# Kernel optimization log

Hardware: AMD Instinct MI355X
Metric: run time of the kernel (lower is better)

The kernel has to match this reference:

```python
import jax, jax.numpy as jnp
import numpy as np

B, S, D = 8, 2048, 768
DK = 768
OUT = 10
EPS = 1e-5

def _layernorm(x, w, b):
    mu = jnp.mean(x, axis=-1, keepdims=True)
    var = jnp.mean(jnp.square(x - mu), axis=-1, keepdims=True)
    return (x - mu) * jax.lax.rsqrt(var + EPS) * w + b

def setup_inputs() -> dict:
    key = jax.random.key(0)
    ks = jax.random.split(key, 8)
    sc_in = 1.0 / np.sqrt(D)
    sc_k = 1.0 / np.sqrt(DK)
    return {
        "src": jax.random.normal(ks[0], (B, S, D), dtype=jnp.float32),
        # weights stored as [in, out] so y = x @ W (equivalent to torch x @ W.T)
        "Wq": jax.random.uniform(ks[1], (D, DK), jnp.float32, -sc_in, sc_in),
        "Wk": jax.random.uniform(ks[2], (D, DK), jnp.float32, -sc_in, sc_in),
        "Wv": jax.random.uniform(ks[3], (D, DK), jnp.float32, -sc_in, sc_in),
        "Wo": jax.random.uniform(ks[4], (DK, D), jnp.float32, -sc_k, sc_k),
        "bo": jnp.zeros((D,), jnp.float32),
        "ln1_w": jnp.ones((D,), jnp.float32),
        "ln1_b": jnp.zeros((D,), jnp.float32),
        "ln2_w": jnp.ones((D,), jnp.float32),
        "ln2_b": jnp.zeros((D,), jnp.float32),
        "Wc": jax.random.uniform(ks[5], (D, OUT), jnp.float32, -sc_in, sc_in),
        "bc": jnp.zeros((OUT,), jnp.float32),
    }

def reference(src, Wq, Wk, Wv, Wo, bo, ln1_w, ln1_b, ln2_w, ln2_b, Wc, bc):
    # Attention (dropout in eval mode -> identity)
    Q = src @ Wq  # [B,S,DK]
    K = src @ Wk
    V = src @ Wv
    scores = jnp.einsum('bsd,btd->bst', Q, K) * (DK ** -0.5)
    attn = jax.nn.softmax(scores, axis=-1)
    out = jnp.einsum('bst,btd->bsd', attn, V) @ Wo + bo
    x = src + out
    x = _layernorm(x, ln1_w, ln1_b)
    x = _layernorm(x, ln2_w, ln2_b)
    pooled = jnp.mean(x, axis=1)  # [B,D]
    logits = pooled @ Wc + bc     # [B,OUT]
    return (logits, x)
```

## Files before the change

### kernel.cpp

```cpp
#include <hip/hip_runtime.h>
#include <cmath>

typedef unsigned short ushort_t;
typedef __bf16 bf16x8 __attribute__((ext_vector_type(8)));
typedef float  f32x4  __attribute__((ext_vector_type(4)));

#define B_  8
#define S_  2048
#define D_  768
#define MROWS (B_ * S_)
#define EPS 1e-5f
#define LDST 40

__device__ __forceinline__ float b2f(ushort_t u) {
    union { unsigned int i; float f; } v; v.i = ((unsigned int)u) << 16; return v.f;
}
__device__ __forceinline__ ushort_t f2b(float f) {
    union { float f; unsigned int i; } v; v.f = f;
    unsigned int r = v.i + 0x7fffu + ((v.i >> 16) & 1u);
    return (ushort_t)(r >> 16);
}

__device__ __forceinline__ void gload16(const ushort_t* g, ushort_t* l) {
    __builtin_amdgcn_global_load_lds((__attribute__((address_space(1))) void*)g,
                                     (__attribute__((address_space(3))) void*)l,
                                     16, 0, 0);
}

__global__ void cast_f32_bf16(const float* __restrict__ in, ushort_t* __restrict__ outp, long n)
{
    const long i = ((long)blockIdx.x * 256 + threadIdx.x) * 4;
    if (i + 3 < n) {
        const float4 v = *(const float4*)(in + i);
        ushort4 o;
        o.x = f2b(v.x); o.y = f2b(v.y); o.z = f2b(v.z); o.w = f2b(v.w);
        *(ushort4*)(outp + i) = o;
    }
}

template<int F32IN>
__global__ void transpose_any(const void* __restrict__ srcv, ushort_t* __restrict__ dst,
                              int R, int C, long sb, long db)
{
    __shared__ ushort_t tile[64 * 65];
    dst += (long)blockIdx.z * db;
    const int r0 = blockIdx.y * 64, c0 = blockIdx.x * 64;
    const int t = threadIdx.x;
    const int tr = t >> 6, tc = t & 63;
    #pragma unroll
    for (int i = 0; i < 16; i++) {
        const int r = i * 4 + tr;
        ushort_t v;
        if (F32IN) v = f2b(((const float*)srcv + (long)blockIdx.z * sb)[(long)(r0 + r) * C + (c0 + tc)]);
        else       v = ((const ushort_t*)srcv + (long)blockIdx.z * sb)[(long)(r0 + r) * C + (c0 + tc)];
        tile[r * 65 + tc] = v;
    }
    __syncthreads();
    #pragma unroll
    for (int i = 0; i < 16; i++) {
        const int r = i * 4 + tr;
        dst[(long)(c0 + r) * R + (r0 + tc)] = tile[tc * 65 + r];
    }
}


__device__ __forceinline__ void stage_half256(const ushort_t* __restrict__ g, int row0,
                                              int Kd, int k0, ushort_t* l, int tid)
{
    #pragma unroll
    for (int i = 0; i < 2; i++) {
        const int c   = i * 512 + tid;
        const int row = c >> 3;
        const int scol = ((c & 7) ^ (row & 7)) * 8;
        gload16(g + (long)(row0 + row) * Kd + (k0 + scol), l + c * 8);
    }
}

#define G256_BAR() do { \
    asm volatile("" ::: "memory"); \
    __builtin_amdgcn_s_barrier(); \
    asm volatile("" ::: "memory"); \
} while (0)

#define G256_LGKM0() asm volatile("s_waitcnt lgkmcnt(0)" ::: "memory")

#define G256_READ_A(q) do { \
    _Pragma("unroll") \
    for (int m2 = 0; m2 < 2; m2++) { \
        _Pragma("unroll") \
        for (int s = 0; s < 2; s++) { \
            int lb = (((q) * 2 + m2) * 16 + r16) * 128 + s * 64 + kq * 16; \
            lb ^= ((lb >> 7) & 7) << 4; \
            af[m2][s] = *reinterpret_cast<const bf16x8*>(LAc + (lb >> 1)); \
        } \
    } \
} while (0)

#define G256_MFMA(q) do { \
    __builtin_amdgcn_s_setprio(1); \
    _Pragma("unroll") \
    for (int m2 = 0; m2 < 2; m2++) { \
        _Pragma("unroll") \
        for (int ni = 0; ni < 4; ni++) { \
            acc[(q) * 2 + m2][ni] = __builtin_amdgcn_mfma_f32_16x16x32_bf16(af[m2][0], bg[ni][0], acc[(q) * 2 + m2][ni], 0, 0, 0); \
            acc[(q) * 2 + m2][ni] = __builtin_amdgcn_mfma_f32_16x16x32_bf16(af[m2][1], bg[ni][1], acc[(q) * 2 + m2][ni], 0, 0, 0); \
        } \
    } \
    __builtin_amdgcn_s_setprio(0); \
} while (0)

template<int MODE>
__global__ __launch_bounds__(512, 2)
void gemm256(const ushort_t* __restrict__ A, const ushort_t* __restrict__ Bt,
             void* __restrict__ Cv, int M, int N, int Kd,
             long batchA, long batchB, long batchC, float scale,
             const float* __restrict__ bias, const float* __restrict__ resid,
             float* __restrict__ rowsum)
{
    __shared__ __align__(16) ushort_t lds[65536];

    const int bz = blockIdx.z;
    A  += (long)bz * batchA;
    Bt += (long)bz * batchB;

    const int nxt  = gridDim.x;
    const int nblk = nxt * gridDim.y;
    int lin = blockIdx.y * nxt + blockIdx.x;
    if ((nblk & 7) == 0) {
        const int per = nblk >> 3;
        lin = (lin & 7) * per + (lin >> 3);
    }
    const int tile_n = (lin % nxt) * 256;
    const int tile_m = (lin / nxt) * 256;

    const int tid  = threadIdx.x;
    const int w    = tid >> 6;
    const int lane = tid & 63;
    const int wr   = w >> 2;
    const int wc   = w & 3;
    const int r16  = lane & 15;
    const int kq   = lane >> 4;
    const int brow = (wc & 1) * 64;

    const int NT = Kd >> 6;

    ushort_t* const sA = lds;
    ushort_t* const sB = lds + 16384;
    const ushort_t* const LA0 = lds + wr * 8192;
    const ushort_t* const LB0 = lds + 16384 + (wc >> 1) * 8192;

    f32x4 acc[8][4] = {};

    stage_half256(A,  tile_m,       Kd, 0,  sA,         tid);
    stage_half256(A,  tile_m + 128, Kd, 0,  sA + 8192,  tid);
    stage_half256(Bt, tile_n,       Kd, 0,  sB,         tid);
    stage_half256(Bt, tile_n + 128, Kd, 0,  sB + 8192,  tid);
    if (NT > 1) {
        stage_half256(Bt, tile_n,       Kd, 64, sB + 32768,        tid);
        stage_half256(Bt, tile_n + 128, Kd, 64, sB + 32768 + 8192, tid);
        asm volatile("s_waitcnt vmcnt(4)" ::: "memory");
    } else {
        asm volatile("s_waitcnt vmcnt(0)" ::: "memory");
    }
    G256_BAR();

    int cur = 0;
    for (int t = 0; t < NT; ++t) {
        const int k0 = t << 6;
        const ushort_t* LAc = LA0 + cur * 32768;
        const ushort_t* LBc = LB0 + cur * 32768;
        ushort_t* const nA  = sA + (cur ^ 1) * 32768;
        ushort_t* const nB  = sB + cur * 32768;

        bf16x8 bg[4][2], af[2][2];

        #pragma unroll
        for (int ni = 0; ni < 4; ni++)
            #pragma unroll
            for (int s = 0; s < 2; s++) {
                int lb = (brow + ni * 16 + r16) * 128 + s * 64 + kq * 16;
                lb ^= ((lb >> 7) & 7) << 4;
                bg[ni][s] = *reinterpret_cast<const bf16x8*>(LBc + (lb >> 1));
            }
        G256_READ_A(0);
        if (t + 1 < NT) stage_half256(A, tile_m, Kd, k0 + 64, nA, tid);
        G256_BAR();
        G256_LGKM0();
        G256_MFMA(0);
        G256_BAR();

        G256_READ_A(1);
        if (t + 1 < NT) stage_half256(A, tile_m + 128, Kd, k0 + 64, nA + 8192, tid);
        G256_BAR();
        G256_LGKM0();
        G256_MFMA(1);
        G256_BAR();

        G256_READ_A(2);
        if (t + 2 < NT) stage_half256(Bt, tile_n, Kd, k0 + 128, nB, tid);
        G256_BAR();
        G256_LGKM0();
        G256_MFMA(2);
        G256_BAR();

        G256_READ_A(3);
        if (t + 2 < NT) stage_half256(Bt, tile_n + 128, Kd, k0 + 128, nB + 8192, tid);
        G256_BAR();
        G256_LGKM0();
        G256_MFMA(3);
        if (t + 2 < NT) { asm volatile("s_waitcnt vmcnt(4)" ::: "memory"); }
        else            { asm volatile("s_waitcnt vmcnt(0)" ::: "memory"); }
        G256_BAR();
        cur ^= 1;
    }

    if (MODE == 1) {
        float* C = (float*)Cv;
        #pragma unroll
        for (int mi = 0; mi < 8; mi++)
            #pragma unroll
            for (int ni = 0; ni < 4; ni++)
                #pragma unroll
                for (int r = 0; r < 4; r++) {
                    const int row = tile_m + wr * 128 + mi * 16 + kq * 4 + r;
                    const int col = tile_n + wc * 64 + ni * 16 + r16;
                    C[(long)row * N + col] =
                        acc[mi][ni][r] + bias[col] + resid[(long)row * N + col];
                }
    } else if (MODE == 2) {
        ushort_t* C = (ushort_t*)Cv + (long)bz * batchC;
        const float* rs = rowsum + (long)bz * 2048;
        #pragma unroll
        for (int mi = 0; mi < 8; mi++) {
            float inv[4];
            #pragma unroll
            for (int r = 0; r < 4; r++)
                inv[r] = 1.0f / rs[tile_m + wr * 128 + mi * 16 + kq * 4 + r];
            #pragma unroll
            for (int ni = 0; ni < 4; ni++)
                #pragma unroll
                for (int r = 0; r < 4; r++) {
                    const int row = tile_m + wr * 128 + mi * 16 + kq * 4 + r;
                    const int col = tile_n + wc * 64 + ni * 16 + r16;
                    C[(long)row * N + col] = f2b(acc[mi][ni][r] * inv[r]);
                }
        }
    } else if (MODE == 3) {
        ushort_t* C = (ushort_t*)Cv + (long)bz * batchC;
        float* rs = rowsum + (long)bz * 2048;
        #pragma unroll
        for (int mi = 0; mi < 8; mi++)
            #pragma unroll
            for (int r = 0; r < 4; r++) {
                const int row = tile_m + wr * 128 + mi * 16 + kq * 4 + r;
                float psum = 0.f;
                #pragma unroll
                for (int ni = 0; ni < 4; ni++) {
                    const float e = __expf(acc[mi][ni][r] * scale);
                    psum += e;
                    const int col = tile_n + wc * 64 + ni * 16 + r16;
                    C[(long)row * N + col] = f2b(e);
                }
                psum += __shfl_xor(psum, 1);
                psum += __shfl_xor(psum, 2);
                psum += __shfl_xor(psum, 4);
                psum += __shfl_xor(psum, 8);
                if (r16 == 0) atomicAdd(&rs[row], psum);
            }
    } else {
        const int sect  = tile_n / 768;
        const int ncol0 = tile_n - sect * 768;
        ushort_t* C = (ushort_t*)Cv + (size_t)sect * ((size_t)MROWS * 768);
        const float sc = (sect == 0) ? scale : 1.0f;
        #pragma unroll
        for (int mi = 0; mi < 8; mi++)
            #pragma unroll
            for (int ni = 0; ni < 4; ni++)
                #pragma unroll
                for (int r = 0; r < 4; r++) {
                    const int row = tile_m + wr * 128 + mi * 16 + kq * 4 + r;
                    const int col = ncol0 + wc * 64 + ni * 16 + r16;
                    C[(long)row * 768 + col] = f2b(acc[mi][ni][r] * sc);
                }
    }
}

template<int MODE>
__global__ __launch_bounds__(256)
void gemm_nt(const ushort_t* __restrict__ A, const ushort_t* __restrict__ Bt,
             void* __restrict__ Cv, int M, int N, int Kd,
             long batchA, long batchB, long batchC, float scale,
             const float* __restrict__ bias, const float* __restrict__ resid,
             float* __restrict__ rowsum)
{
    __shared__ __align__(16) ushort_t As[128 * 32];
    __shared__ __align__(16) ushort_t Bs[128 * 32];

    const int bz = blockIdx.z;
    A  += (long)bz * batchA;
    Bt += (long)bz * batchB;

    const int nxt  = gridDim.x;
    const int nblk = nxt * gridDim.y;
    int lin = blockIdx.y * nxt + blockIdx.x;
    if ((nblk & 7) == 0) {
        const int per = nblk >> 3;
        lin = (lin & 7) * per + (lin >> 3);
    }
    const int tile_n = (lin % nxt) * 128;
    const int tile_m = (lin / nxt) * 128;

    const int tid  = threadIdx.x;
    const int w    = tid >> 6;
    const int lane = tid & 63;
    const int wr = w >> 1, wc = w & 1;
    const int r16 = lane & 15;
    const int kq  = lane >> 4;

    const int srow   = lane >> 2;
    const int schunk = lane & 3;
    const int arow0 = w * 32 + srow;
    const int arow1 = arow0 + 16;
    const int g0 = (schunk ^ ((arow0 >> 1) & 3)) * 8;
    const int g1 = (schunk ^ ((arow1 >> 1) & 3)) * 8;

    const ushort_t* Ar0 = A  + (long)(tile_m + arow0) * Kd + g0;
    const ushort_t* Ar1 = A  + (long)(tile_m + arow1) * Kd + g1;
    const ushort_t* Br0 = Bt + (long)(tile_n + arow0) * Kd + g0;
    const ushort_t* Br1 = Bt + (long)(tile_n + arow1) * Kd + g1;

    ushort_t* lA0 = &As[(w * 32     ) * 32];
    ushort_t* lA1 = &As[(w * 32 + 16) * 32];
    ushort_t* lB0 = &Bs[(w * 32     ) * 32];
    ushort_t* lB1 = &Bs[(w * 32 + 16) * 32];

    f32x4 acc[4][4] = {};

    for (int k0 = 0; k0 < Kd; k0 += 32) {
        gload16(Ar0 + k0, lA0);
        gload16(Ar1 + k0, lA1);
        gload16(Br0 + k0, lB0);
        gload16(Br1 + k0, lB1);
        __syncthreads();

        bf16x8 af[4], bg[4];
        #pragma unroll
        for (int i = 0; i < 4; i++) {
            const int ra = wr * 64 + i * 16 + r16;
            af[i] = *reinterpret_cast<const bf16x8*>(&As[ra * 32 + ((kq ^ ((ra >> 1) & 3)) * 8)]);
            const int rb = wc * 64 + i * 16 + r16;
            bg[i] = *reinterpret_cast<const bf16x8*>(&Bs[rb * 32 + ((kq ^ ((rb >> 1) & 3)) * 8)]);
        }
        #pragma unroll
        for (int mi = 0; mi < 4; mi++)
            #pragma unroll
            for (int ni = 0; ni < 4; ni++)
                acc[mi][ni] = __builtin_amdgcn_mfma_f32_16x16x32_bf16(af[mi], bg[ni], acc[mi][ni], 0, 0, 0);
        __syncthreads();
    }

    if (MODE == 0) {
        ushort_t* C = (ushort_t*)Cv + (long)bz * batchC;
        #pragma unroll
        for (int mi = 0; mi < 4; mi++)
            #pragma unroll
            for (int ni = 0; ni < 4; ni++)
                #pragma unroll
                for (int r = 0; r < 4; r++) {
                    const int row = tile_m + wr * 64 + mi * 16 + kq * 4 + r;
                    const int col = tile_n + wc * 64 + ni * 16 + r16;
                    C[(long)row * N + col] = f2b(acc[mi][ni][r] * scale);
                }
    } else if (MODE == 1) {
        float* C = (float*)Cv;
        #pragma unroll
        for (int mi = 0; mi < 4; mi++)
            #pragma unroll
            for (int ni = 0; ni < 4; ni++)
                #pragma unroll
                for (int r = 0; r < 4; r++) {
                    const int row = tile_m + wr * 64 + mi * 16 + kq * 4 + r;
                    const int col = tile_n + wc * 64 + ni * 16 + r16;
                    C[(long)row * N + col] =
                        acc[mi][ni][r] + bias[col] + resid[(long)row * N + col];
                }
    } else if (MODE == 2) {
        ushort_t* C = (ushort_t*)Cv + (long)bz * batchC;
        const float* rs = rowsum + (long)bz * 2048;
        #pragma unroll
        for (int mi = 0; mi < 4; mi++) {
            float inv[4];
            #pragma unroll
            for (int r = 0; r < 4; r++)
                inv[r] = 1.0f / rs[tile_m + wr * 64 + mi * 16 + kq * 4 + r];
            #pragma unroll
            for (int ni = 0; ni < 4; ni++)
                #pragma unroll
                for (int r = 0; r < 4; r++) {
                    const int row = tile_m + wr * 64 + mi * 16 + kq * 4 + r;
                    const int col = tile_n + wc * 64 + ni * 16 + r16;
                    C[(long)row * N + col] = f2b(acc[mi][ni][r] * inv[r]);
                }
        }
    } else if (MODE == 3) {
        ushort_t* C = (ushort_t*)Cv + (long)bz * batchC;
        float* rs = rowsum + (long)bz * 2048;
        #pragma unroll
        for (int mi = 0; mi < 4; mi++)
            #pragma unroll
            for (int r = 0; r < 4; r++) {
                const int row = tile_m + wr * 64 + mi * 16 + kq * 4 + r;
                float psum = 0.f;
                #pragma unroll
                for (int ni = 0; ni < 4; ni++) {
                    const float e = __expf(acc[mi][ni][r] * scale);
                    psum += e;
                    const int col = tile_n + wc * 64 + ni * 16 + r16;
                    C[(long)row * N + col] = f2b(e);
                }
                psum += __shfl_xor(psum, 1);
                psum += __shfl_xor(psum, 2);
                psum += __shfl_xor(psum, 4);
                psum += __shfl_xor(psum, 8);
                if (r16 == 0) atomicAdd(&rs[row], psum);
            }
    } else {
        const int sect  = tile_n / 768;
        const int ncol0 = tile_n - sect * 768;
        ushort_t* C = (ushort_t*)Cv + (size_t)sect * ((size_t)MROWS * 768);
        const float sc = (sect == 0) ? scale : 1.0f;
        #pragma unroll
        for (int mi = 0; mi < 4; mi++)
            #pragma unroll
            for (int ni = 0; ni < 4; ni++)
                #pragma unroll
                for (int r = 0; r < 4; r++) {
                    const int row = tile_m + wr * 64 + mi * 16 + kq * 4 + r;
                    const int col = ncol0 + wc * 64 + ni * 16 + r16;
                    C[(long)row * 768 + col] = f2b(acc[mi][ni][r] * sc);
                }
    }
}

template<int TRANSB, int MODE, int BF32>
__global__ __launch_bounds__(256)
void gemm_s(const ushort_t* __restrict__ A, const void* __restrict__ Bsrc,
            void* __restrict__ Cv, int M, int N, int Kd, float scale,
            const float* __restrict__ bias, const float* __restrict__ resid)
{
    __shared__ __align__(16) ushort_t As[128 * LDST];
    __shared__ __align__(16) ushort_t Bs[128 * LDST];
    const int tile_n = blockIdx.x * 128;
    const int tile_m = blockIdx.y * 128;
    const int tid  = threadIdx.x;
    const int w    = tid >> 6;
    const int lane = tid & 63;
    const int wr = w >> 1, wc = w & 1;
    const int r16 = lane & 15;
    const int kq  = lane >> 4;
    f32x4 acc[4][4] = {};
    for (int k0 = 0; k0 < Kd; k0 += 32) {
        #pragma unroll
        for (int cc = 0; cc < 2; cc++) {
            const int c = tid + cc * 256;
            const int row = c >> 2, col = (c & 3) * 8;
            *(uint4*)&As[row * LDST + col] = *(const uint4*)(A + (long)(tile_m + row) * Kd + k0 + col);
        }
        if (TRANSB == 0) {
            const ushort_t* Bt = (const ushort_t*)Bsrc;
            #pragma unroll
            for (int cc = 0; cc < 2; cc++) {
                const int c = tid + cc * 256;
                const int row = c >> 2, col = (c & 3) * 8;
                *(uint4*)&Bs[row * LDST + col] = *(const uint4*)(Bt + (long)(tile_n + row) * Kd + k0 + col);
            }
        } else {
            #pragma unroll
            for (int i = 0; i < 16; i++) {
                const int lin = i * 256 + tid;
                const int kr = lin >> 7, nc = lin & 127;
                ushort_t bv;
                if (BF32) bv = f2b(((const float*)Bsrc)[(long)(k0 + kr) * N + tile_n + nc]);
                else      bv = ((const ushort_t*)Bsrc)[(long)(k0 + kr) * N + tile_n + nc];
                Bs[nc * LDST + kr] = bv;
            }
        }
        __syncthreads();
        bf16x8 af[4], bg[4];
        #pragma unroll
        for (int i = 0; i < 4; i++) {
            af[i] = *reinterpret_cast<const bf16x8*>(&As[(wr * 64 + i * 16 + r16) * LDST + kq * 8]);
            bg[i] = *reinterpret_cast<const bf16x8*>(&Bs[(wc * 64 + i * 16 + r16) * LDST + kq * 8]);
        }
        #pragma unroll
        for (int mi = 0; mi < 4; mi++)
            #pragma unroll
            for (int ni = 0; ni < 4; ni++)
                acc[mi][ni] = __builtin_amdgcn_mfma_f32_16x16x32_bf16(af[mi], bg[ni], acc[mi][ni], 0, 0, 0);
        __syncthreads();
    }
    if (MODE == 0) {
        ushort_t* C = (ushort_t*)Cv;
        #pragma unroll
        for (int mi = 0; mi < 4; mi++)
            #pragma unroll
            for (int ni = 0; ni < 4; ni++)
                #pragma unroll
                for (int r = 0; r < 4; r++) {
                    const int row = tile_m + wr * 64 + mi * 16 + kq * 4 + r;
                    const int col = tile_n + wc * 64 + ni * 16 + r16;
                    C[(long)row * N + col] = f2b(acc[mi][ni][r] * scale);
                }
    } else {
        float* C = (float*)Cv;
        #pragma unroll
        for (int mi = 0; mi < 4; mi++)
            #pragma unroll
            for (int ni = 0; ni < 4; ni++)
                #pragma unroll
                for (int r = 0; r < 4; r++) {
                    const int row = tile_m + wr * 64 + mi * 16 + kq * 4 + r;
                    const int col = tile_n + wc * 64 + ni * 16 + r16;
                    C[(long)row * N + col] =
                        acc[mi][ni][r] + bias[col] + resid[(long)row * N + col];
                }
    }
}

__global__ void softmax_rows(ushort_t* __restrict__ p)
{
    __shared__ float sm[4], ss_[4];
    ushort_t* pr = p + (long)blockIdx.x * 2048;
    const int tid = threadIdx.x;
    const int w = tid >> 6;
    const uint4 raw = *(const uint4*)(pr + tid * 8);
    float v[8];
    v[0] = b2f((ushort_t)(raw.x & 0xffff)); v[1] = b2f((ushort_t)(raw.x >> 16));
    v[2] = b2f((ushort_t)(raw.y & 0xffff)); v[3] = b2f((ushort_t)(raw.y >> 16));
    v[4] = b2f((ushort_t)(raw.z & 0xffff)); v[5] = b2f((ushort_t)(raw.z >> 16));
    v[6] = b2f((ushort_t)(raw.w & 0xffff)); v[7] = b2f((ushort_t)(raw.w >> 16));
    float mx = -3.0e38f;
    #pragma unroll
    for (int i = 0; i < 8; i++) mx = fmaxf(mx, v[i]);
    #pragma unroll
    for (int off = 32; off; off >>= 1) mx = fmaxf(mx, __shfl_xor(mx, off));
    if ((tid & 63) == 0) sm[w] = mx;
    __syncthreads();
    mx = fmaxf(fmaxf(sm[0], sm[1]), fmaxf(sm[2], sm[3]));
    float s = 0.f;
    #pragma unroll
    for (int i = 0; i < 8; i++) { v[i] = __expf(v[i] - mx); s += v[i]; }
    #pragma unroll
    for (int off = 32; off; off >>= 1) s += __shfl_xor(s, off);
    if ((tid & 63) == 0) ss_[w] = s;
    __syncthreads();
    s = ss_[0] + ss_[1] + ss_[2] + ss_[3];
    const float inv = 1.f / s;
    uint4 o;
    o.x = f2b(v[0] * inv) | ((unsigned)f2b(v[1] * inv) << 16);
    o.y = f2b(v[2] * inv) | ((unsigned)f2b(v[3] * inv) << 16);
    o.z = f2b(v[4] * inv) | ((unsigned)f2b(v[5] * inv) << 16);
    o.w = f2b(v[6] * inv) | ((unsigned)f2b(v[7] * inv) << 16);
    *(uint4*)(pr + tid * 8) = o;
}

__global__ void ln_fused(float* __restrict__ x,
                         const float* __restrict__ w1, const float* __restrict__ b1,
                         const float* __restrict__ w2, const float* __restrict__ b2)
{
    __shared__ float r1s[4], r1q[4], r2s[4], r2q[4];
    const long row = blockIdx.x;
    const int tid = threadIdx.x;
    const int w = tid >> 6;
    float* xr = x + row * 768;
    float v[3], s = 0.f, q = 0.f;
    #pragma unroll
    for (int i = 0; i < 3; i++) { const float t = xr[tid + i * 256]; v[i] = t; s += t; q += t * t; }
    #pragma unroll
    for (int off = 32; off; off >>= 1) { s += __shfl_xor(s, off); q += __shfl_xor(q, off); }
    if ((tid & 63) == 0) { r1s[w] = s; r1q[w] = q; }
    __syncthreads();
    s = r1s[0] + r1s[1] + r1s[2] + r1s[3];
    q = r1q[0] + r1q[1] + r1q[2] + r1q[3];
    float mu = s * (1.f / 768.f);
    float ri = rsqrtf(q * (1.f / 768.f) - mu * mu + EPS);
    float y[3];
    s = 0.f; q = 0.f;
    #pragma unroll
    for (int i = 0; i < 3; i++) {
        const int d = tid + i * 256;
        const float t = (v[i] - mu) * ri * w1[d] + b1[d];
        y[i] = t; s += t; q += t * t;
    }
    #pragma unroll
    for (int off = 32; off; off >>= 1) { s += __shfl_xor(s, off); q += __shfl_xor(q, off); }
    if ((tid & 63) == 0) { r2s[w] = s; r2q[w] = q; }
    __syncthreads();
    s = r2s[0] + r2s[1] + r2s[2] + r2s[3];
    q = r2q[0] + r2q[1] + r2q[2] + r2q[3];
    mu = s * (1.f / 768.f);
    ri = rsqrtf(q * (1.f / 768.f) - mu * mu + EPS);
    #pragma unroll
    for (int i = 0; i < 3; i++) {
        const int d = tid + i * 256;
        xr[d] = (y[i] - mu) * ri * w2[d] + b2[d];
    }
}

__global__ void pool_reduce(const float* __restrict__ x, float* __restrict__ pooled)
{
    const int d  = blockIdx.x * 256 + threadIdx.x;
    const int b  = blockIdx.z;
    const int sp = blockIdx.y;
    const float* base = x + ((long)b * 2048 + sp * 128) * 768 + d;
    float s = 0.f;
    #pragma unroll 8
    for (int i = 0; i < 128; i++) s += base[(long)i * 768];
    atomicAdd(&pooled[b * 768 + d], s);
}

__global__ void logits_kernel(const float* __restrict__ pooled, const float* __restrict__ Wc,
                              const float* __restrict__ bc, float* __restrict__ out)
{
    const int b = blockIdx.x / 10, o = blockIdx.x % 10;
    const int lane = threadIdx.x;
    float s = 0.f;
    #pragma unroll
    for (int d = lane; d < 768; d += 64) s += pooled[b * 768 + d] * Wc[d * 10 + o];
    #pragma unroll
    for (int off = 32; off; off >>= 1) s += __shfl_xor(s, off);
    if (lane == 0) out[b * 10 + o] = s * (1.f / 2048.f) + bc[o];
}

extern "C" void kernel_launch(void* const* d_in, const int* in_sizes, int n_in,
                              void* d_out, int out_size, void* d_ws, size_t ws_size,
                              hipStream_t stream)
{
    (void)in_sizes; (void)n_in; (void)out_size;
    const float* src  = (const float*)d_in[0];
    const float* Wq   = (const float*)d_in[1];
    const float* Wk   = (const float*)d_in[2];
    const float* Wv   = (const float*)d_in[3];
    const float* Wo   = (const float*)d_in[4];
    const float* bo   = (const float*)d_in[5];
    const float* ln1w = (const float*)d_in[6];
    const float* ln1b = (const float*)d_in[7];
    const float* ln2w = (const float*)d_in[8];
    const float* ln2b = (const float*)d_in[9];
    const float* Wc   = (const float*)d_in[10];
    const float* bc   = (const float*)d_in[11];
    float* out = (float*)d_out;

    const dim3 blk(256);
    const dim3 blk512(512);
    const float qscale = 1.0f / sqrtf(768.0f);
    const long bs = (long)2048 * 768;

    const size_t WT    = (size_t)768 * 768 * 2;
    const size_t BUF   = (size_t)MROWS * 768 * 2;
    const size_t POOLB = 24576;
    const size_t RSB   = (size_t)B_ * 2048 * 4;
    const size_t PROBS8 = (size_t)8 * 2048 * 2048 * 2;
    const size_t needB = 4 * WT + 5 * BUF + POOLB + RSB;
    const size_t needA = needB + PROBS8;

    char* ws = (char*)d_ws;
    size_t off = 0;
    auto alloc = [&](size_t bytes) { void* p = ws + off; off += (bytes + 255) & ~(size_t)255; return p; };

    if (ws_size >= needB) {
        ushort_t* Wtq  = (ushort_t*)alloc(WT);
        ushort_t* Wtk  = (ushort_t*)alloc(WT);
        ushort_t* Wtv  = (ushort_t*)alloc(WT);
        ushort_t* Wto  = (ushort_t*)alloc(WT);
        ushort_t* srcb = (ushort_t*)alloc(BUF);
        ushort_t* Qb   = (ushort_t*)alloc(BUF);
        ushort_t* Kb   = (ushort_t*)alloc(BUF);
        ushort_t* Vb   = (ushort_t*)alloc(BUF);
        ushort_t* Vt   = (ushort_t*)alloc(BUF);
        float*  pooled = (float*)  alloc(POOLB);
        float*  rowsum = (float*)  alloc(RSB);
        const bool batched = (ws_size >= needA);
        ushort_t* probs = batched ? (ushort_t*)alloc(PROBS8) : srcb;
        ushort_t* attn  = Vb;
        float*    xpre  = out + 80;

        cast_f32_bf16<<<MROWS * 768 / 1024, blk, 0, stream>>>(src, srcb, (long)MROWS * 768);
        transpose_any<1><<<dim3(12, 12, 1), blk, 0, stream>>>(Wq, Wtq, 768, 768, 0, 0);
        transpose_any<1><<<dim3(12, 12, 1), blk, 0, stream>>>(Wk, Wtk, 768, 768, 0, 0);
        transpose_any<1><<<dim3(12, 12, 1), blk, 0, stream>>>(Wv, Wtv, 768, 768, 0, 0);
        transpose_any<1><<<dim3(12, 12, 1), blk, 0, stream>>>(Wo, Wto, 768, 768, 0, 0);

        gemm256<4><<<dim3(9, 64, 1), blk512, 0, stream>>>(srcb, Wtq, Qb, MROWS, 2304, 768,
                                                          0, 0, 0, qscale, nullptr, nullptr, nullptr);

        transpose_any<0><<<dim3(12, 32, B_), blk, 0, stream>>>(Vb, Vt, 2048, 768, bs, bs);
        hipMemsetAsync(rowsum, 0, RSB, stream);

        if (batched) {
            gemm256<3><<<dim3(8, 8, B_), blk512, 0, stream>>>(Qb, Kb, probs, 2048, 2048, 768,
                                                              bs, bs, (long)2048 * 2048, 1.0f,
                                                              nullptr, nullptr, rowsum);
            gemm256<2><<<dim3(3, 8, B_), blk512, 0, stream>>>(probs, Vt, attn, 2048, 768, 2048,
                                                              (long)2048 * 2048, bs, bs, 1.0f,
                                                              nullptr, nullptr, rowsum);
        } else {
            for (int bz = 0; bz < B_; bz += 2) {
                gemm_nt<3><<<dim3(16, 16, 2), blk, 0, stream>>>(Qb + bz * bs, Kb + bz * bs, probs,
                                                                2048, 2048, 768, bs, bs, (long)2048 * 2048,
                                                                1.0f, nullptr, nullptr, rowsum + bz * 2048);
                gemm_nt<2><<<dim3(6, 16, 2), blk, 0, stream>>>(probs, Vt + bz * bs, attn + bz * bs,
                                                               2048, 768, 2048,
                                                               (long)2048 * 2048, bs, bs, 1.0f,
                                                               nullptr, nullptr, rowsum + bz * 2048);
            }
        }

        gemm256<1><<<dim3(3, 64, 1), blk512, 0, stream>>>(attn, Wto, xpre, MROWS, 768, 768,
                                                          0, 0, 0, 1.0f, bo, src, nullptr);
        ln_fused<<<MROWS, blk, 0, stream>>>(xpre, ln1w, ln1b, ln2w, ln2b);
        hipMemsetAsync(pooled, 0, B_ * 768 * 4, stream);
        pool_reduce<<<dim3(3, 16, B_), blk, 0, stream>>>(xpre, pooled);
        logits_kernel<<<80, 64, 0, stream>>>(pooled, Wc, bc, out);
    } else {
        ushort_t* srcb = (ushort_t*)alloc(BUF);
        ushort_t* Qb   = (ushort_t*)alloc(BUF);
        ushort_t* Kb   = (ushort_t*)alloc(BUF);
        ushort_t* Vb   = (ushort_t*)alloc(BUF);
        float*  pooled = (float*)  alloc(POOLB);
        ushort_t* probs = srcb;
        ushort_t* attn  = Qb;
        float*    xpre  = out + 80;

        cast_f32_bf16<<<MROWS * 768 / 1024, blk, 0, stream>>>(src, srcb, (long)MROWS * 768);
        gemm_s<1, 0, 1><<<dim3(6, 128), blk, 0, stream>>>(srcb, Wq, Qb, MROWS, 768, 768, qscale, nullptr, nullptr);
        gemm_s<1, 0, 1><<<dim3(6, 128), blk, 0, stream>>>(srcb, Wk, Kb, MROWS, 768, 768, 1.0f, nullptr, nullptr);
        gemm_s<1, 0, 1><<<dim3(6, 128), blk, 0, stream>>>(srcb, Wv, Vb, MROWS, 768, 768, 1.0f, nullptr, nullptr);
        for (int bz = 0; bz < B_; bz++) {
            gemm_s<0, 0, 0><<<dim3(16, 16), blk, 0, stream>>>(Qb + bz * bs, Kb + bz * bs, probs,
                                                              2048, 2048, 768, 1.0f, nullptr, nullptr);
            softmax_rows<<<2048, blk, 0, stream>>>(probs);
            gemm_s<1, 0, 0><<<dim3(6, 16), blk, 0, stream>>>(probs, Vb + bz * bs, attn + bz * bs,
                                                             2048, 768, 2048, 1.0f, nullptr, nullptr);
        }
        gemm_s<1, 1, 1><<<dim3(6, 128), blk, 0, stream>>>(attn, Wo, xpre, MROWS, 768, 768, 1.0f, bo, src);
        ln_fused<<<MROWS, blk, 0, stream>>>(xpre, ln1w, ln1b, ln2w, ln2b);
        hipMemsetAsync(pooled, 0, B_ * 768 * 4, stream);
        pool_reduce<<<dim3(3, 16, B_), blk, 0, stream>>>(xpre, pooled);
        logits_kernel<<<80, 64, 0, stream>>>(pooled, Wc, bc, out);
    }
}
```

Baseline: 441.5 us.

## Fuse V transpose into QKV epilogue, pooling into layernorm, precompute staging offsets

The QKV GEMM epilogue now writes the V section straight into a transposed [B, D, S] layout using 4-wide stores, which removes the separate transpose kernel. Layernorm now accumulates the pooled sum with per-element atomics, replacing the pool_reduce kernel. The GEMM staging address math is hoisted into precomputed per-thread offsets, and an extra lgkmcnt wait is added. The per-element atomics (16K rows × 768) may contend heavily, and the transposed V stores are strided by 2048 elements.

```diff
diff --git a/kernel.cpp b/kernel.cpp
--- a/kernel.cpp
+++ b/kernel.cpp
@@ -63,18 +63,6 @@
     }
 }
 
-
-__device__ __forceinline__ void stage_half256(const ushort_t* __restrict__ g, int row0,
-                                              int Kd, int k0, ushort_t* l, int tid)
-{
-    #pragma unroll
-    for (int i = 0; i < 2; i++) {
-        const int c   = i * 512 + tid;
-        const int row = c >> 3;
-        const int scol = ((c & 7) ^ (row & 7)) * 8;
-        gload16(g + (long)(row0 + row) * Kd + (k0 + scol), l + c * 8);
-    }
-}
 
 #define G256_BAR() do { \
     asm volatile("" ::: "memory"); \
@@ -144,6 +132,18 @@
 
     const int NT = Kd >> 6;
 
+    const int c0 = tid, c1 = tid + 512;
+    const long aoff0 = (long)(c0 >> 3) * Kd + (((c0 & 7) ^ ((c0 >> 3) & 7)) << 3);
+    const long aoff1 = (long)(c1 >> 3) * Kd + (((c1 & 7) ^ ((c1 >> 3) & 7)) << 3);
+    const ushort_t* const Ag = A + (long)tile_m * Kd;
+    const ushort_t* const Bg = Bt + (long)tile_n * Kd;
+    const long KHALF = (long)128 * Kd;
+
+    auto STAGE = [&](const ushort_t* gb, long disp, ushort_t* l) {
+        gload16(gb + disp + aoff0, l + c0 * 8);
+        gload16(gb + disp + aoff1, l + c1 * 8);
+    };
+
     ushort_t* const sA = lds;
     ushort_t* const sB = lds + 16384;
     const ushort_t* const LA0 = lds + wr * 8192;
@@ -151,13 +151,13 @@
 
     f32x4 acc[8][4] = {};
 
-    stage_half256(A,  tile_m,       Kd, 0,  sA,         tid);
-    stage_half256(A,  tile_m + 128, Kd, 0,  sA + 8192,  tid);
-    stage_half256(Bt, tile_n,       Kd, 0,  sB,         tid);
-    stage_half256(Bt, tile_n + 128, Kd, 0,  sB + 8192,  tid);
+    STAGE(Ag, 0,     sA);
+    STAGE(Ag, KHALF, sA + 8192);
+    STAGE(Bg, 0,     sB);
+    STAGE(Bg, KHALF, sB + 8192);
     if (NT > 1) {
-        stage_half256(Bt, tile_n,       Kd, 64, sB + 32768,        tid);
-        stage_half256(Bt, tile_n + 128, Kd, 64, sB + 32768 + 8192, tid);
+        STAGE(Bg, 64,         sB + 32768);
+        STAGE(Bg, KHALF + 64, sB + 32768 + 8192);
         asm volatile("s_waitcnt vmcnt(4)" ::: "memory");
     } else {
         asm volatile("s_waitcnt vmcnt(0)" ::: "memory");
@@ -166,7 +166,7 @@
 
     int cur = 0;
     for (int t = 0; t < NT; ++t) {
-        const int k0 = t << 6;
+        const long k0 = (long)(t << 6);
         const ushort_t* LAc = LA0 + cur * 32768;
         const ushort_t* LBc = LB0 + cur * 32768;
         ushort_t* const nA  = sA + (cur ^ 1) * 32768;
@@ -183,28 +183,29 @@
                 bg[ni][s] = *reinterpret_cast<const bf16x8*>(LBc + (lb >> 1));
             }
         G256_READ_A(0);
-        if (t + 1 < NT) stage_half256(A, tile_m, Kd, k0 + 64, nA, tid);
+        if (t + 1 < NT) STAGE(Ag, k0 + 64, nA);
+        asm volatile("s_waitcnt lgkmcnt(8)" ::: "memory");
         G256_BAR();
         G256_LGKM0();
         G256_MFMA(0);
         G256_BAR();
 
         G256_READ_A(1);
-        if (t + 1 < NT) stage_half256(A, tile_m + 128, Kd, k0 + 64, nA + 8192, tid);
+        if (t + 1 < NT) STAGE(Ag, KHALF + k0 + 64, nA + 8192);
         G256_BAR();
         G256_LGKM0();
         G256_MFMA(1);
         G256_BAR();
 
         G256_READ_A(2);
-        if (t + 2 < NT) stage_half256(Bt, tile_n, Kd, k0 + 128, nB, tid);
+        if (t + 2 < NT) STAGE(Bg, k0 + 128, nB);
         G256_BAR();
         G256_LGKM0();
         G256_MFMA(2);
         G256_BAR();
 
         G256_READ_A(3);
-        if (t + 2 < NT) stage_half256(Bt, tile_n + 128, Kd, k0 + 128, nB + 8192, tid);
+        if (t + 2 < NT) STAGE(Bg, KHALF + k0 + 128, nB + 8192);
         G256_BAR();
         G256_LGKM0();
         G256_MFMA(3);
@@ -270,18 +271,34 @@
     } else {
         const int sect  = tile_n / 768;
         const int ncol0 = tile_n - sect * 768;
-        ushort_t* C = (ushort_t*)Cv + (size_t)sect * ((size_t)MROWS * 768);
-        const float sc = (sect == 0) ? scale : 1.0f;
-        #pragma unroll
-        for (int mi = 0; mi < 8; mi++)
-            #pragma unroll
-            for (int ni = 0; ni < 4; ni++)
-                #pragma unroll
-                for (int r = 0; r < 4; r++) {
-                    const int row = tile_m + wr * 128 + mi * 16 + kq * 4 + r;
-                    const int col = ncol0 + wc * 64 + ni * 16 + r16;
-                    C[(long)row * 768 + col] = f2b(acc[mi][ni][r] * sc);
-                }
+        if (sect == 2) {
+            ushort_t* Vt = (ushort_t*)rowsum;
+            #pragma unroll
+            for (int mi = 0; mi < 8; mi++)
+                #pragma unroll
+                for (int ni = 0; ni < 4; ni++) {
+                    const int row = tile_m + wr * 128 + mi * 16 + kq * 4;
+                    const int d   = ncol0 + wc * 64 + ni * 16 + r16;
+                    const int b   = row >> 11, s = row & 2047;
+                    ushort4 o;
+                    o.x = f2b(acc[mi][ni][0]); o.y = f2b(acc[mi][ni][1]);
+                    o.z = f2b(acc[mi][ni][2]); o.w = f2b(acc[mi][ni][3]);
+                    *(ushort4*)(Vt + (long)b * ((long)2048 * 768) + (long)d * 2048 + s) = o;
+                }
+        } else {
+            ushort_t* C = (ushort_t*)Cv + (size_t)sect * ((size_t)MROWS * 768);
+            const float sc = (sect == 0) ? scale : 1.0f;
+            #pragma unroll
+            for (int mi = 0; mi < 8; mi++)
+                #pragma unroll
+                for (int ni = 0; ni < 4; ni++)
+                    #pragma unroll
+                    for (int r = 0; r < 4; r++) {
+                        const int row = tile_m + wr * 128 + mi * 16 + kq * 4 + r;
+                        const int col = ncol0 + wc * 64 + ni * 16 + r16;
+                        C[(long)row * 768 + col] = f2b(acc[mi][ni][r] * sc);
+                    }
+        }
     }
 }
 
@@ -566,12 +583,14 @@
 
 __global__ void ln_fused(float* __restrict__ x,
                          const float* __restrict__ w1, const float* __restrict__ b1,
-                         const float* __restrict__ w2, const float* __restrict__ b2)
+                         const float* __restrict__ w2, const float* __restrict__ b2,
+                         float* __restrict__ pooled)
 {
     __shared__ float r1s[4], r1q[4], r2s[4], r2q[4];
     const long row = blockIdx.x;
     const int tid = threadIdx.x;
     const int w = tid >> 6;
+    const int b = (int)(row >> 11);
     float* xr = x + row * 768;
     float v[3], s = 0.f, q = 0.f;
     #pragma unroll
@@ -603,20 +622,10 @@
     #pragma unroll
     for (int i = 0; i < 3; i++) {
         const int d = tid + i * 256;
-        xr[d] = (y[i] - mu) * ri * w2[d] + b2[d];
-    }
-}
-
-__global__ void pool_reduce(const float* __restrict__ x, float* __restrict__ pooled)
-{
-    const int d  = blockIdx.x * 256 + threadIdx.x;
-    const int b  = blockIdx.z;
-    const int sp = blockIdx.y;
-    const float* base = x + ((long)b * 2048 + sp * 128) * 768 + d;
-    float s = 0.f;
-    #pragma unroll 8
-    for (int i = 0; i < 128; i++) s += base[(long)i * 768];
-    atomicAdd(&pooled[b * 768 + d], s);
+        const float val = (y[i] - mu) * ri * w2[d] + b2[d];
+        xr[d] = val;
+        atomicAdd(&pooled[b * 768 + d], val);
+    }
 }
 
 __global__ void logits_kernel(const float* __restrict__ pooled, const float* __restrict__ Wc,
@@ -692,9 +701,8 @@
         transpose_any<1><<<dim3(12, 12, 1), blk, 0, stream>>>(Wo, Wto, 768, 768, 0, 0);
 
         gemm256<4><<<dim3(9, 64, 1), blk512, 0, stream>>>(srcb, Wtq, Qb, MROWS, 2304, 768,
-                                                          0, 0, 0, qscale, nullptr, nullptr, nullptr);
-
-        transpose_any<0><<<dim3(12, 32, B_), blk, 0, stream>>>(Vb, Vt, 2048, 768, bs, bs);
+                                                          0, 0, 0, qscale, nullptr, nullptr, (float*)Vt);
+
         hipMemsetAsync(rowsum, 0, RSB, stream);
 
         if (batched) {
@@ -718,9 +726,8 @@
 
         gemm256<1><<<dim3(3, 64, 1), blk512, 0, stream>>>(attn, Wto, xpre, MROWS, 768, 768,
                                                           0, 0, 0, 1.0f, bo, src, nullptr);
-        ln_fused<<<MROWS, blk, 0, stream>>>(xpre, ln1w, ln1b, ln2w, ln2b);
         hipMemsetAsync(pooled, 0, B_ * 768 * 4, stream);
-        pool_reduce<<<dim3(3, 16, B_), blk, 0, stream>>>(xpre, pooled);
+        ln_fused<<<MROWS, blk, 0, stream>>>(xpre, ln1w, ln1b, ln2w, ln2b, pooled);
         logits_kernel<<<80, 64, 0, stream>>>(pooled, Wc, bc, out);
     } else {
         ushort_t* srcb = (ushort_t*)alloc(BUF);
@@ -744,9 +751,8 @@
                                                              2048, 768, 2048, 1.0f, nullptr, nullptr);
         }
         gemm_s<1, 1, 1><<<dim3(6, 128), blk, 0, stream>>>(attn, Wo, xpre, MROWS, 768, 768, 1.0f, bo, src);
-        ln_fused<<<MROWS, blk, 0, stream>>>(xpre, ln1w, ln1b, ln2w, ln2b);
         hipMemsetAsync(pooled, 0, B_ * 768 * 4, stream);
-        pool_reduce<<<dim3(3, 16, B_), blk, 0, stream>>>(xpre, pooled);
+        ln_fused<<<MROWS, blk, 0, stream>>>(xpre, ln1w, ln1b, ln2w, ln2b, pooled);
         logits_kernel<<<80, 64, 0, stream>>>(pooled, Wc, bc, out);
     }
 }
```

New measurement: 558.8 us. 1.27x slower.
